# Optimization experiments

Measured on AMD Instinct MI355X. Metric: run time of the kernel, lower is better.

Reference implementation:

```python
import math
import jax, jax.numpy as jnp
import numpy as np

N = 50000      # nodes
E = 800000     # edges
H = 128        # hidden_dim
NR = 16        # num_radial
CUTOFF = 5.0
LN_EPS = 1e-5


def _ln(h, g, b):
    m = jnp.mean(h, axis=-1, keepdims=True)
    v = jnp.mean((h - m) ** 2, axis=-1, keepdims=True)
    return (h - m) * jax.lax.rsqrt(v + LN_EPS) * g + b


def _legendre(angle):
    # degree=4 -> 4 polynomial features
    c = jnp.cos(angle)
    p0 = jnp.ones_like(c)
    p1 = c
    p2 = (3.0 * c * p1 - 1.0 * p0) / 2.0
    p3 = (5.0 * c * p2 - 2.0 * p1) / 3.0
    return jnp.concatenate([p0, p1, p2, p3], axis=-1)


def setup_inputs() -> dict:
    key = jax.random.key(0)
    ks = jax.random.split(key, 16)
    ED = 2 * H + NR + 3  # edge feature dim = 275

    def w(k, shape, fan_in):
        return jax.random.normal(k, shape, jnp.float32) / np.sqrt(fan_in).astype(np.float32)

    return {
        "x": jax.random.normal(ks[0], (N, H), jnp.float32),
        "pos": jax.random.normal(ks[1], (N, 3), jnp.float32),
        "charge": jax.random.normal(ks[2], (N, 1), jnp.float32),
        "edge_attr": jax.random.uniform(ks[3], (E, 4), jnp.float32),
        "edge_index": jax.random.randint(ks[4], (2, E), 0, N),
        "We1": w(ks[5], (ED, H), ED), "be1": jnp.zeros((H,), jnp.float32),
        "g1": jnp.ones((H,), jnp.float32), "bt1": jnp.zeros((H,), jnp.float32),
        "We2": w(ks[6], (H, H), H), "be2": jnp.zeros((H,), jnp.float32),
        "Wn": w(ks[7], (2 * H, H), 2 * H), "bn": jnp.zeros((H,), jnp.float32),
        "gn": jnp.ones((H,), jnp.float32), "btn": jnp.zeros((H,), jnp.float32),
        "Wc1": w(ks[8], (H, H // 2), H), "bc1": jnp.zeros((H // 2,), jnp.float32),
        "Wc2": w(ks[9], (H // 2, 1), H // 2), "bc2": jnp.zeros((1,), jnp.float32),
    }


def reference(x, pos, charge, edge_attr, edge_index,
              We1, be1, g1, bt1, We2, be2, Wn, bn, gn, btn,
              Wc1, bc1, Wc2, bc2):
    src, dst = edge_index[0], edge_index[1]

    rel = pos[dst] - pos[src]                                   # [E,3]
    dist = jnp.sqrt(jnp.sum(rel ** 2, axis=-1, keepdims=True) + 1e-8)
    unit = rel / jnp.clip(dist, 1e-6)

    # edge-attribute gate via Legendre basis of angle/dihedral
    af = _legendre(edge_attr[:, 0:1])
    df = _legendre(edge_attr[:, 1:2])
    a_score = jnp.mean(jnp.abs(af), axis=-1, keepdims=True) * edge_attr[:, 2:3]
    d_score = jnp.mean(jnp.abs(df), axis=-1, keepdims=True) * edge_attr[:, 3:4]
    gate = jnp.clip(1.0 + 0.6 * (a_score + d_score), 0.35, 2.5)  # [E,1]

    # spherical Bessel radial basis
    freq = jnp.arange(1, NR + 1, dtype=jnp.float32) * (math.pi / CUTOFF)
    clipped = jnp.clip(dist, 1e-6)
    rad = jnp.sin(freq * clipped) / clipped                      # [E,NR]

    qs, qd = charge[src], charge[dst]
    ef = jnp.concatenate([
        x[src], x[dst], rad * gate, dist / CUTOFF * gate,
        qs * qd * gate, jnp.abs(qs - qd) * gate], axis=-1)       # [E,275]

    h = jax.nn.silu(ef @ We1 + be1)
    h = _ln(h, g1, bt1)
    eh = jax.nn.silu(h @ We2 + be2)                              # [E,H]

    ones = jnp.ones((eh.shape[0], 1), eh.dtype)
    cnt = jnp.clip(jax.ops.segment_sum(ones, src, num_segments=N), 1.0)
    agg = jax.ops.segment_sum(eh, src, num_segments=N) / cnt     # scatter-mean

    coord = jax.nn.silu(eh @ Wc1 + bc1) @ Wc2 + bc2              # [E,1]
    delta = jax.ops.segment_sum(unit * coord * gate, src, num_segments=N) / cnt

    x_new = x + _ln(jax.nn.silu(jnp.concatenate([x, agg], axis=-1) @ Wn + bn), gn, btn)
    pos_new = pos + 0.1 * delta
    return (x_new, pos_new)
```

## Files before the change

kernel.cpp:

```cpp
#include <hip/hip_runtime.h>
#include <hip/hip_bf16.h>
#include <math.h>


#define HDIM 128
#define GN   16
#define TILE 64
#define HS   136
#define AUXS 32
#define NS   264

#define B_BE1 0
#define B_G1  128
#define B_BT1 256
#define B_BE2 384
#define B_BC1 512
#define B_WC2 576
#define B_BC2 640
#define B_BN  704
#define B_GN  832
#define B_BTN 960
#define BIAS_N 1088

typedef unsigned int uint32;
typedef float f32x4 __attribute__((ext_vector_type(4)));
typedef float f32x2 __attribute__((ext_vector_type(2)));
typedef short short8 __attribute__((ext_vector_type(8)));
typedef unsigned short u16x4 __attribute__((ext_vector_type(4)));

__device__ __forceinline__ float bf2f(__hip_bfloat16 h) { return __bfloat162float(h); }

template<bool BF> __device__ __forceinline__ f32x2 ld2(const void* p, size_t i) {
  if constexpr (BF) {
    uint32 u; __builtin_memcpy(&u, (const char*)p + i * 2, 4);
    f32x2 r; r.x = __uint_as_float(u << 16); r.y = __uint_as_float(u & 0xffff0000u);
    return r;
  } else {
    f32x2 r; __builtin_memcpy(&r, (const char*)p + i * 4, 8);
    return r;
  }
}
template<bool BF> __device__ __forceinline__ float ld1(const void* p, size_t i) {
  if constexpr (BF) {
    __hip_bfloat16 h; __builtin_memcpy(&h, (const char*)p + i * 2, 2);
    return bf2f(h);
  } else {
    float v; __builtin_memcpy(&v, (const char*)p + i * 4, 4);
    return v;
  }
}
template<bool BF> __device__ __forceinline__ void st1(void* p, size_t i, float v) {
  if constexpr (BF) {
    __hip_bfloat16 h = __float2bfloat16(v);
    __builtin_memcpy((char*)p + i * 2, &h, 2);
  } else {
    __builtin_memcpy((char*)p + i * 4, &v, 4);
  }
}

__device__ __forceinline__ unsigned short f2bf(float v) {
  __hip_bfloat16 h = __float2bfloat16(v);
  unsigned short u; __builtin_memcpy(&u, &h, 2);
  return u;
}

template<bool BF> __device__ __forceinline__ f32x4 ld4(const void* p, size_t i) {
  if constexpr (BF) {
    u16x4 u; __builtin_memcpy(&u, (const char*)p + i * 2, 8);
    f32x4 r;
    r.x = __uint_as_float((uint32)u[0] << 16);
    r.y = __uint_as_float((uint32)u[1] << 16);
    r.z = __uint_as_float((uint32)u[2] << 16);
    r.w = __uint_as_float((uint32)u[3] << 16);
    return r;
  } else {
    f32x4 r; __builtin_memcpy(&r, (const char*)p + i * 4, 16);
    return r;
  }
}

template<bool BF> __device__ __forceinline__ short8 ldxrow(const void* x, int row, int col) {
  if constexpr (BF) {
    return *reinterpret_cast<const short8*>((const char*)x + ((size_t)row * HDIM + col) * 2);
  } else {
    const float* p = (const float*)x + (size_t)row * HDIM + col;
    f32x4 v0 = *reinterpret_cast<const f32x4*>(p);
    f32x4 v1 = *reinterpret_cast<const f32x4*>(p + 4);
    short8 a;
    a[0] = (short)f2bf(v0.x); a[1] = (short)f2bf(v0.y);
    a[2] = (short)f2bf(v0.z); a[3] = (short)f2bf(v0.w);
    a[4] = (short)f2bf(v1.x); a[5] = (short)f2bf(v1.y);
    a[6] = (short)f2bf(v1.z); a[7] = (short)f2bf(v1.w);
    return a;
  }
}

__device__ __forceinline__ float silu(float v) { return v / (1.0f + __expf(-v)); }

__device__ __forceinline__ f32x4 splat4(float v) {
  f32x4 r; r.x = v; r.y = v; r.z = v; r.w = v; return r;
}

__device__ __forceinline__ void wave_sync() {
  asm volatile("s_waitcnt lgkmcnt(0)" ::: "memory");
}

__global__ void probe_kernel(const uint32* g1, int* flag) {
  if (threadIdx.x == 0 && blockIdx.x == 0) *flag = (g1[0] == 0x3F800000u) ? 0 : 1;
}

__global__ void hist_kernel(const int* __restrict__ ei, int* __restrict__ cnt, int E) {
  int e = blockIdx.x * 256 + threadIdx.x;
  if (e < E) atomicAdd(&cnt[ei[e]], 1);
}

__global__ void __launch_bounds__(1024) scan_kernel(const int* __restrict__ cnt,
                                                    int* __restrict__ off, int N) {
  __shared__ int part[16];
  __shared__ int carry_s;
  const int t = threadIdx.x;
  const int wid = t >> 6, ln = t & 63;
  if (t == 0) carry_s = 0;
  __syncthreads();
  for (int base = 0; base < N; base += 1024) {
    const int v = (base + t < N) ? cnt[base + t] : 0;
    int inc = v;
#pragma unroll
    for (int s = 1; s < 64; s <<= 1) {
      int u = __shfl_up(inc, s);
      if (ln >= s) inc += u;
    }
    if (ln == 63) part[wid] = inc;
    __syncthreads();
    if (wid == 0) {
      int p = (ln < 16) ? part[ln] : 0;
#pragma unroll
      for (int s = 1; s < 16; s <<= 1) {
        int u = __shfl_up(p, s);
        if (ln >= s) p += u;
      }
      if (ln < 16) part[ln] = p;
    }
    __syncthreads();
    const int woff = (wid > 0) ? part[wid - 1] : 0;
    const int carry = carry_s;
    if (base + t < N) off[base + t] = carry + inc + woff - v;
    __syncthreads();
    if (t == 1023) carry_s = carry + part[15];
    __syncthreads();
  }
  if (t == 0) off[N] = carry_s;
}

__global__ void fill_kernel(const int* __restrict__ ei, const int* __restrict__ off,
                            int* __restrict__ cursor, int* __restrict__ eidx, int E) {
  int e = blockIdx.x * 256 + threadIdx.x;
  if (e < E) {
    int s = ei[e];
    int p = atomicAdd(&cursor[s], 1);
    eidx[off[s] + p] = e;
  }
}

template<bool BF>
__global__ void __launch_bounds__(256) prep_kernel(
    const void* __restrict__ x,
    const void* __restrict__ pos, const void* __restrict__ charge,
    const void* __restrict__ We1, const void* __restrict__ We2,
    const void* __restrict__ Wc1, const void* __restrict__ Wn,
    const void* __restrict__ be1, const void* __restrict__ g1,
    const void* __restrict__ bt1, const void* __restrict__ be2,
    const void* __restrict__ bc1, const void* __restrict__ wc2,
    const void* __restrict__ bc2, const void* __restrict__ bn,
    const void* __restrict__ gn, const void* __restrict__ btn,
    const int* __restrict__ flag,
    float* __restrict__ posf, float* __restrict__ chgf, float* __restrict__ biasf,
    __hip_bfloat16* __restrict__ WT1, __hip_bfloat16* __restrict__ WT2,
    __hip_bfloat16* __restrict__ WTc1, __hip_bfloat16* __restrict__ WTn,
    __hip_bfloat16* __restrict__ xbf,
    int N) {
  if (*flag != (BF ? 1 : 0)) return;
  const int gt = blockIdx.x * 256 + threadIdx.x;
  const int gs = gridDim.x * 256;
  for (int i = gt; i < N * 3; i += gs) posf[i] = ld1<BF>(pos, i);
  for (int i = gt; i < N; i += gs) chgf[i] = ld1<BF>(charge, i);
  if (xbf) {
    for (int i = gt; i < N * HDIM; i += gs) xbf[i] = __float2bfloat16(ld1<BF>(x, i));
  }
  for (int i = gt; i < 128; i += gs) {
    biasf[B_BE1 + i] = ld1<BF>(be1, i);
    biasf[B_G1  + i] = ld1<BF>(g1, i);
    biasf[B_BT1 + i] = ld1<BF>(bt1, i);
    biasf[B_BE2 + i] = ld1<BF>(be2, i);
    biasf[B_BN  + i] = ld1<BF>(bn, i);
    biasf[B_GN  + i] = ld1<BF>(gn, i);
    biasf[B_BTN + i] = ld1<BF>(btn, i);
  }
  for (int i = gt; i < 64; i += gs) {
    biasf[B_BC1 + i] = ld1<BF>(bc1, i);
    biasf[B_WC2 + i] = ld1<BF>(wc2, i);
  }
  if (gt == 0) biasf[B_BC2] = ld1<BF>(bc2, 0);
  for (int i = gt; i < 128 * 288; i += gs) {
    int n = i / 288, k = i % 288;
    float v = (k < 275) ? ld1<BF>(We1, (size_t)k * 128 + n) : 0.f;
    WT1[i] = __float2bfloat16(v);
  }
  for (int i = gt; i < 128 * 128; i += gs) {
    int n = i / 128, k = i % 128;
    WT2[i] = __float2bfloat16(ld1<BF>(We2, (size_t)k * 128 + n));
  }
  for (int i = gt; i < 64 * 128; i += gs) {
    int n = i / 128, k = i % 128;
    WTc1[i] = __float2bfloat16(ld1<BF>(Wc1, (size_t)k * 64 + n));
  }
  for (int i = gt; i < 128 * 256; i += gs) {
    int n = i / 256, k = i % 256;
    WTn[i] = __float2bfloat16(ld1<BF>(Wn, (size_t)k * 128 + n));
  }
}

template<bool BF, bool XB>
__global__ void __launch_bounds__(256, 2) edge_mfma_kernel(
    const void* __restrict__ x, const void* __restrict__ eattr,
    const int* __restrict__ ei,
    const int* __restrict__ off, const int* __restrict__ eidx,
    const int* __restrict__ flag,
    const float* __restrict__ posf, const float* __restrict__ chgf,
    const float* __restrict__ biasf,
    const __hip_bfloat16* __restrict__ WT1, const __hip_bfloat16* __restrict__ WT2,
    const __hip_bfloat16* __restrict__ WTc1, const __hip_bfloat16* __restrict__ WTn,
    const __hip_bfloat16* __restrict__ xbf,
    void* __restrict__ out, int N, int E) {
  if (*flag != (BF ? 1 : 0)) return;

  __shared__ __align__(16) __hip_bfloat16 hbuf[4 * 16 * HS];
  __shared__ __align__(16) __hip_bfloat16 aux_s[TILE * AUXS];
  __shared__ float base_s[GN * 132];
  __shared__ float agg_s[(GN + 1) * 132];
  __shared__ float dsum_s[(GN + 1) * 4];
  __shared__ float sgate[TILE];
  __shared__ float sunit[TILE * 3];
  __shared__ int sdst_s[TILE];
  __shared__ int offs[GN + 1];
  __shared__ short ssrc16[TILE];

  const int tid = threadIdx.x;
  const int w = tid >> 6;
  const int lane = tid & 63;
  const int g0 = blockIdx.x * GN;
  const int c16 = lane & 15;
  const int g4 = lane >> 4;

  for (int i = tid; i < (GN + 1) * 132; i += 256) agg_s[i] = 0.f;
  for (int i = tid; i < (GN + 1) * 4; i += 256) dsum_s[i] = 0.f;
  if (tid <= GN) {
    int node = g0 + tid;
    offs[tid] = off[node < N ? node : N];
  }
  __syncthreads();

  const int eStart = offs[0];
  const int eEnd = offs[GN];
  const int ntiles = (eEnd - eStart + TILE - 1) / TILE;

  __hip_bfloat16* hw = hbuf + (size_t)w * 16 * HS;

  const short* WT1s = reinterpret_cast<const short*>(WT1);
  const short* WT2s = reinterpret_cast<const short*>(WT2);
  const short* WTc1s = reinterpret_cast<const short*>(WTc1);
  const short* xbs = reinterpret_cast<const short*>(xbf);

  {
    for (int i = tid; i < GN * 32; i += 256) {
      const int row = i >> 5, c4 = (i & 31) * 4;
      int node = g0 + row; node = (node < N) ? node : (N - 1);
      if constexpr (XB) {
        *reinterpret_cast<u16x4*>(&hbuf[row * HS + c4]) =
            *reinterpret_cast<const u16x4*>(&xbs[(size_t)node * HDIM + c4]);
      } else {
        const size_t xb = (size_t)node * HDIM + c4;
        f32x2 v0 = ld2<BF>(x, xb);
        f32x2 v1 = ld2<BF>(x, xb + 2);
        u16x4 pk;
        pk[0] = f2bf(v0.x); pk[1] = f2bf(v0.y); pk[2] = f2bf(v1.x); pk[3] = f2bf(v1.y);
        *reinterpret_cast<u16x4*>(&hbuf[row * HS + c4]) = pk;
      }
    }
    __syncthreads();
    f32x4 acc2[2];
#pragma unroll
    for (int j = 0; j < 2; j++)
      acc2[j] = splat4(biasf[B_BE1 + (2 * w + j) * 16 + c16]);
#pragma unroll
    for (int ks = 0; ks < 4; ks++) {
      short8 a = *reinterpret_cast<const short8*>(&hbuf[c16 * HS + ks * 32 + g4 * 8]);
#pragma unroll
      for (int j = 0; j < 2; j++) {
        const int nt = 2 * w + j;
        short8 b = *reinterpret_cast<const short8*>(
            &WT1s[(size_t)(nt * 16 + c16) * 288 + ks * 32 + g4 * 8]);
        acc2[j] = __builtin_amdgcn_mfma_f32_16x16x32_bf16(a, b, acc2[j], 0, 0, 0);
      }
    }
#pragma unroll
    for (int j = 0; j < 2; j++) {
      const int nt = 2 * w + j;
#pragma unroll
      for (int r = 0; r < 4; r++)
        base_s[(g4 * 4 + r) * 132 + nt * 16 + c16] = acc2[j][r];
    }
    __syncthreads();
  }

  const float FSC = 3.14159265358979323846f / 5.0f;

  const int es_pl = lane >> 2;
  int pos_cur = eStart + w * 16 + es_pl;
  bool v_cur = (ntiles > 0) && (pos_cur < eEnd);
  int eg_cur = v_cur ? eidx[pos_cur] : 0;
  int dst_cur = v_cur ? ei[(size_t)E + eg_cur] : g0;

  for (int t = 0; t < ntiles; t++) {
    const int pos_nx = pos_cur + TILE;
    const bool v_nx = pos_nx < eEnd;
    const int eg_nx = v_nx ? eidx[pos_nx] : 0;

    {
      const int es = es_pl, sub = lane & 3, slot = w * 16 + es;
      const bool valid = v_cur;
      int loc = GN;
      if (valid) {
        loc = 0;
#pragma unroll
        for (int st = 8; st > 0; st >>= 1)
          if (loc + st <= GN - 1 && offs[loc + st] <= pos_cur) loc += st;
      }
      const int dstn = dst_cur;
      float gate = 0.f, dcl = 1.f, ux = 0.f, uy = 0.f, uz = 0.f;
      float f0 = 0.f, f1 = 0.f, f2 = 0.f;
      if (valid && sub == 0) {
        const int srcg = g0 + loc;
        const float px = posf[3 * srcg + 0], py = posf[3 * srcg + 1], pz = posf[3 * srcg + 2];
        const float qn = chgf[srcg];
        const float dx = posf[3 * dstn + 0] - px;
        const float dy = posf[3 * dstn + 1] - py;
        const float dz = posf[3 * dstn + 2] - pz;
        const float dist = sqrtf(dx * dx + dy * dy + dz * dz + 1e-8f);
        dcl = fmaxf(dist, 1e-6f);
        ux = dx / dcl; uy = dy / dcl; uz = dz / dcl;
        f32x4 ea = ld4<BF>(eattr, (size_t)eg_cur * 4);
        const float ca = __cosf(ea.x);
        const float p2a = 0.5f * (3.f * ca * ca - 1.f);
        const float p3a = (5.f * ca * p2a - 2.f * ca) * (1.f / 3.f);
        const float ma = 0.25f * (1.f + fabsf(ca) + fabsf(p2a) + fabsf(p3a));
        const float cd = __cosf(ea.y);
        const float p2d = 0.5f * (3.f * cd * cd - 1.f);
        const float p3d = (5.f * cd * p2d - 2.f * cd) * (1.f / 3.f);
        const float md = 0.25f * (1.f + fabsf(cd) + fabsf(p2d) + fabsf(p3d));
        gate = fminf(fmaxf(1.f + 0.6f * (ma * ea.z + md * ea.w), 0.35f), 2.5f);
        const float qd = chgf[dstn];
        f0 = dist * 0.2f * gate;
        f1 = qn * qd * gate;
        f2 = fabsf(qn - qd) * gate;
      }
      const int bl = lane & ~3;
      dcl = __shfl(dcl, bl);
      gate = __shfl(gate, bl);
      u16x4 rv;
#pragma unroll
      for (int i = 0; i < 4; i++) {
        const float k1 = (float)(sub * 4 + i + 1);
        rv[i] = f2bf(__sinf(FSC * k1 * dcl) / dcl * gate);
      }
      *reinterpret_cast<u16x4*>(&aux_s[slot * AUXS + sub * 4]) = rv;
      if (sub == 0) {
        sgate[slot] = gate;
        ssrc16[slot] = (short)(valid ? loc : GN);
        sdst_s[slot] = dstn;
        sunit[slot * 3 + 0] = ux; sunit[slot * 3 + 1] = uy;
        sunit[slot * 3 + 2] = uz;
        u16x4 ev;
        ev[0] = f2bf(f0); ev[1] = f2bf(f1); ev[2] = f2bf(f2); ev[3] = 0;
        *reinterpret_cast<u16x4*>(&aux_s[slot * AUXS + 16]) = ev;
      } else {
        u16x4 z; z[0] = 0; z[1] = 0; z[2] = 0; z[3] = 0;
        *reinterpret_cast<u16x4*>(&aux_s[slot * AUXS + 16 + sub * 4]) = z;
      }
    }
    wave_sync();

    int ssr[4];
#pragma unroll
    for (int r = 0; r < 4; r++) ssr[r] = (int)ssrc16[w * 16 + g4 * 4 + r];
    const int dstc = sdst_s[w * 16 + c16];

    f32x4 acc[8];
#pragma unroll
    for (int nt = 0; nt < 8; nt++) {
      f32x4 c;
#pragma unroll
      for (int r = 0; r < 4; r++) {
        const int sb = (ssr[r] < GN) ? ssr[r] : (GN - 1);
        c[r] = base_s[sb * 132 + nt * 16 + c16];
      }
      acc[nt] = c;
    }
#pragma unroll
    for (int ks = 0; ks < 4; ks++) {
      short8 a;
      if constexpr (XB) {
        a = *reinterpret_cast<const short8*>(
            &xbs[(size_t)dstc * HDIM + ks * 32 + g4 * 8]);
      } else {
        a = ldxrow<BF>(x, dstc, ks * 32 + g4 * 8);
      }
#pragma unroll
      for (int nt = 0; nt < 8; nt++) {
        short8 b = *reinterpret_cast<const short8*>(
            &WT1s[(size_t)(nt * 16 + c16) * 288 + 128 + ks * 32 + g4 * 8]);
        acc[nt] = __builtin_amdgcn_mfma_f32_16x16x32_bf16(a, b, acc[nt], 0, 0, 0);
      }
    }
    {
      short8 a = *reinterpret_cast<const short8*>(&aux_s[(w * 16 + c16) * AUXS + g4 * 8]);
#pragma unroll
      for (int nt = 0; nt < 8; nt++) {
        short8 b = *reinterpret_cast<const short8*>(
            &WT1s[(size_t)(nt * 16 + c16) * 288 + 256 + g4 * 8]);
        acc[nt] = __builtin_amdgcn_mfma_f32_16x16x32_bf16(a, b, acc[nt], 0, 0, 0);
      }
    }

    {
      float sm[4] = {0.f, 0.f, 0.f, 0.f}, sq[4] = {0.f, 0.f, 0.f, 0.f};
#pragma unroll
      for (int nt = 0; nt < 8; nt++)
#pragma unroll
        for (int r = 0; r < 4; r++) {
          const float v = silu(acc[nt][r]);
          acc[nt][r] = v;
          sm[r] += v;
          sq[r] += v * v;
        }
#pragma unroll
      for (int r = 0; r < 4; r++) {
#pragma unroll
        for (int mk = 1; mk <= 8; mk <<= 1) {
          sm[r] += __shfl_xor(sm[r], mk);
          sq[r] += __shfl_xor(sq[r], mk);
        }
      }
      float mu[4], rsd[4];
#pragma unroll
      for (int r = 0; r < 4; r++) {
        mu[r] = sm[r] * (1.f / HDIM);
        const float var = sq[r] * (1.f / HDIM) - mu[r] * mu[r];
        rsd[r] = rsqrtf(var + 1e-5f);
      }
#pragma unroll
      for (int nt = 0; nt < 8; nt++) {
        const float gg = biasf[B_G1 + nt * 16 + c16];
        const float bb = biasf[B_BT1 + nt * 16 + c16];
#pragma unroll
        for (int r = 0; r < 4; r++) {
          const int m = g4 * 4 + r;
          hw[m * HS + nt * 16 + c16] =
              __float2bfloat16((acc[nt][r] - mu[r]) * rsd[r] * gg + bb);
        }
      }
    }
    wave_sync();

#pragma unroll
    for (int nt = 0; nt < 8; nt++) acc[nt] = splat4(biasf[B_BE2 + nt * 16 + c16]);
#pragma unroll
    for (int ks = 0; ks < 4; ks++) {
      short8 a = *reinterpret_cast<const short8*>(&hw[c16 * HS + ks * 32 + g4 * 8]);
#pragma unroll
      for (int nt = 0; nt < 8; nt++) {
        short8 b = *reinterpret_cast<const short8*>(
            &WT2s[(size_t)(nt * 16 + c16) * 128 + ks * 32 + g4 * 8]);
        acc[nt] = __builtin_amdgcn_mfma_f32_16x16x32_bf16(a, b, acc[nt], 0, 0, 0);
      }
    }
#pragma unroll
    for (int nt = 0; nt < 8; nt++)
#pragma unroll
      for (int r = 0; r < 4; r++) {
        const float v = silu(acc[nt][r]);
        const int m = g4 * 4 + r;
        hw[m * HS + nt * 16 + c16] = __float2bfloat16(v);
        atomicAdd(&agg_s[ssr[r] * 132 + nt * 16 + c16], v);
      }
    wave_sync();

    {
      f32x4 a3[4];
#pragma unroll
      for (int q = 0; q < 4; q++) a3[q] = splat4(biasf[B_BC1 + q * 16 + c16]);
#pragma unroll
      for (int ks = 0; ks < 4; ks++) {
        short8 a = *reinterpret_cast<const short8*>(&hw[c16 * HS + ks * 32 + g4 * 8]);
#pragma unroll
        for (int q = 0; q < 4; q++) {
          short8 b = *reinterpret_cast<const short8*>(
              &WTc1s[(size_t)(q * 16 + c16) * 128 + ks * 32 + g4 * 8]);
          a3[q] = __builtin_amdgcn_mfma_f32_16x16x32_bf16(a, b, a3[q], 0, 0, 0);
        }
      }
      float cp[4] = {0.f, 0.f, 0.f, 0.f};
#pragma unroll
      for (int q = 0; q < 4; q++) {
        const float wv = biasf[B_WC2 + q * 16 + c16];
#pragma unroll
        for (int r = 0; r < 4; r++) cp[r] += silu(a3[q][r]) * wv;
      }
#pragma unroll
      for (int r = 0; r < 4; r++) {
#pragma unroll
        for (int mk = 1; mk <= 8; mk <<= 1) cp[r] += __shfl_xor(cp[r], mk);
      }
      const float bc2v = biasf[B_BC2];
      if (c16 < 4) {
        const int r = c16;
        const int slot = w * 16 + g4 * 4 + r;
        const float cr = (r == 0) ? cp[0] : (r == 1) ? cp[1] : (r == 2) ? cp[2] : cp[3];
        const float scale = (cr + bc2v) * sgate[slot];
        const int sl = (int)ssrc16[slot];
        atomicAdd(&dsum_s[sl * 4 + 0], sunit[slot * 3 + 0] * scale);
        atomicAdd(&dsum_s[sl * 4 + 1], sunit[slot * 3 + 1] * scale);
        atomicAdd(&dsum_s[sl * 4 + 2], sunit[slot * 3 + 2] * scale);
      }
    }
    wave_sync();

    const int dst_nx = v_nx ? ei[(size_t)E + eg_nx] : g0;
    pos_cur = pos_nx;
    v_cur = v_nx;
    eg_cur = eg_nx;
    dst_cur = dst_nx;
  }
  __syncthreads();

  for (int m = w; m < GN; m += 4) {
    const int node = g0 + m;
    const bool nv = node < N;
    const int dg = nv ? (offs[m + 1] - offs[m]) : 0;
    const float inv = 1.f / fmaxf((float)dg, 1.f);
    const int cb = lane * 4;
    u16x4 pk;
    if (nv && cb < 128) {
      if constexpr (XB) {
        pk = *reinterpret_cast<const u16x4*>(&xbs[(size_t)node * HDIM + cb]);
      } else {
#pragma unroll
        for (int j = 0; j < 4; j++) pk[j] = f2bf(ld1<BF>(x, (size_t)node * HDIM + cb + j));
      }
    } else {
#pragma unroll
      for (int j = 0; j < 4; j++) {
        const int col = cb + j;
        float v = 0.f;
        if (nv && col >= 128) v = agg_s[m * 132 + (col - 128)] * inv;
        pk[j] = f2bf(v);
      }
    }
    *reinterpret_cast<u16x4*>(&hbuf[m * NS + cb]) = pk;
  }
  __syncthreads();

  if (w == 0) {
    const short* WTns = reinterpret_cast<const short*>(WTn);
    f32x4 an[8];
#pragma unroll
    for (int nt = 0; nt < 8; nt++) an[nt] = splat4(biasf[B_BN + nt * 16 + c16]);
#pragma unroll
    for (int ks = 0; ks < 8; ks++) {
      short8 a = *reinterpret_cast<const short8*>(&hbuf[c16 * NS + ks * 32 + g4 * 8]);
#pragma unroll
      for (int nt = 0; nt < 8; nt++) {
        short8 b = *reinterpret_cast<const short8*>(
            &WTns[(size_t)(nt * 16 + c16) * 256 + ks * 32 + g4 * 8]);
        an[nt] = __builtin_amdgcn_mfma_f32_16x16x32_bf16(a, b, an[nt], 0, 0, 0);
      }
    }
    float sm[4] = {0.f, 0.f, 0.f, 0.f}, sq[4] = {0.f, 0.f, 0.f, 0.f};
#pragma unroll
    for (int nt = 0; nt < 8; nt++)
#pragma unroll
      for (int r = 0; r < 4; r++) {
        const float v = silu(an[nt][r]);
        an[nt][r] = v;
        sm[r] += v;
        sq[r] += v * v;
      }
#pragma unroll
    for (int r = 0; r < 4; r++) {
#pragma unroll
      for (int mk = 1; mk <= 8; mk <<= 1) {
        sm[r] += __shfl_xor(sm[r], mk);
        sq[r] += __shfl_xor(sq[r], mk);
      }
    }
    float mu[4], rsd[4];
#pragma unroll
    for (int r = 0; r < 4; r++) {
      mu[r] = sm[r] * (1.f / HDIM);
      const float var = sq[r] * (1.f / HDIM) - mu[r] * mu[r];
      rsd[r] = rsqrtf(var + 1e-5f);
    }
#pragma unroll
    for (int nt = 0; nt < 8; nt++) {
      const float gg = biasf[B_GN + nt * 16 + c16];
      const float bb = biasf[B_BTN + nt * 16 + c16];
#pragma unroll
      for (int r = 0; r < 4; r++) {
        const int m = g4 * 4 + r;
        const int node = g0 + m;
        if (node < N) {
          const int col = nt * 16 + c16;
          const float xo = ld1<BF>(x, (size_t)node * HDIM + col);
          st1<BF>(out, (size_t)node * HDIM + col,
                  xo + (an[nt][r] - mu[r]) * rsd[r] * gg + bb);
        }
      }
    }
    if (lane < GN) {
      const int node = g0 + lane;
      if (node < N) {
        const int dg = offs[lane + 1] - offs[lane];
        const float inv = 1.f / fmaxf((float)dg, 1.f);
#pragma unroll
        for (int d = 0; d < 3; d++) {
          const float pv = posf[(size_t)node * 3 + d] + 0.1f * dsum_s[lane * 4 + d] * inv;
          st1<BF>(out, (size_t)N * HDIM + (size_t)node * 3 + d, pv);
        }
      }
    }
  }
}

extern "C" void kernel_launch(void* const* d_in, const int* in_sizes, int n_in,
                              void* d_out, int out_size, void* d_ws, size_t ws_size,
                              hipStream_t stream) {
  const void* x      = d_in[0];
  const void* pos    = d_in[1];
  const void* charge = d_in[2];
  const void* eattr  = d_in[3];
  const int*  ei     = (const int*)d_in[4];
  const void* We1 = d_in[5];  const void* be1 = d_in[6];
  const void* g1  = d_in[7];  const void* bt1 = d_in[8];
  const void* We2 = d_in[9];  const void* be2 = d_in[10];
  const void* Wn  = d_in[11]; const void* bn  = d_in[12];
  const void* gn  = d_in[13]; const void* btn = d_in[14];
  const void* Wc1 = d_in[15]; const void* bc1 = d_in[16];
  const void* Wc2 = d_in[17]; const void* bc2 = d_in[18];

  const int N = in_sizes[0] / HDIM;
  const int E = in_sizes[3] / 4;

  int* wsI    = (int*)d_ws;
  int* flag   = wsI;
  int* cnt    = wsI + 1;
  int* cursor = cnt + N;
  int* off    = cursor + N;
  int* eidx   = off + (N + 1);

  char* base = (char*)d_ws;
  size_t o = ((size_t)(3 * N + 2 + E) * 4 + 511) & ~(size_t)511;
  float* posf = (float*)(base + o);
  o = (o + (size_t)N * 3 * 4 + 511) & ~(size_t)511;
  float* chgf = (float*)(base + o);
  o = (o + (size_t)N * 4 + 511) & ~(size_t)511;
  float* biasf = (float*)(base + o);
  o = (o + (size_t)BIAS_N * 4 + 511) & ~(size_t)511;
  __hip_bfloat16* WT1 = (__hip_bfloat16*)(base + o);
  o = (o + (size_t)128 * 288 * 2 + 511) & ~(size_t)511;
  __hip_bfloat16* WT2 = (__hip_bfloat16*)(base + o);
  o = (o + (size_t)128 * 128 * 2 + 511) & ~(size_t)511;
  __hip_bfloat16* WTc1 = (__hip_bfloat16*)(base + o);
  o = (o + (size_t)64 * 128 * 2 + 511) & ~(size_t)511;
  __hip_bfloat16* WTn = (__hip_bfloat16*)(base + o);
  o = (o + (size_t)128 * 256 * 2 + 511) & ~(size_t)511;
  __hip_bfloat16* xbf_ws = (__hip_bfloat16*)(base + o);
  const bool xb_fits = (o + (size_t)N * HDIM * 2) <= ws_size;

  hipMemsetAsync(d_ws, 0, (size_t)(1 + 2 * N) * sizeof(int), stream);

  probe_kernel<<<1, 64, 0, stream>>>((const uint32*)g1, flag);

  const int eb = (E + 255) / 256;
  hist_kernel<<<eb, 256, 0, stream>>>(ei, cnt, E);
  scan_kernel<<<1, 1024, 0, stream>>>(cnt, off, N);
  fill_kernel<<<eb, 256, 0, stream>>>(ei, off, cursor, eidx, E);

  prep_kernel<true><<<512, 256, 0, stream>>>(
      x, pos, charge, We1, We2, Wc1, Wn, be1, g1, bt1, be2, bc1, Wc2, bc2, bn, gn, btn,
      flag, posf, chgf, biasf, WT1, WT2, WTc1, WTn, nullptr, N);
  prep_kernel<false><<<512, 256, 0, stream>>>(
      x, pos, charge, We1, We2, Wc1, Wn, be1, g1, bt1, be2, bc1, Wc2, bc2, bn, gn, btn,
      flag, posf, chgf, biasf, WT1, WT2, WTc1, WTn, xb_fits ? xbf_ws : nullptr, N);

  const int nb = (N + GN - 1) / GN;
  edge_mfma_kernel<true, true><<<nb, 256, 0, stream>>>(
      x, eattr, ei, off, eidx, flag, posf, chgf, biasf, WT1, WT2, WTc1, WTn,
      (const __hip_bfloat16*)x, d_out, N, E);
  if (xb_fits) {
    edge_mfma_kernel<false, true><<<nb, 256, 0, stream>>>(
        x, eattr, ei, off, eidx, flag, posf, chgf, biasf, WT1, WT2, WTc1, WTn,
        xbf_ws, d_out, N, E);
  } else {
    edge_mfma_kernel<false, false><<<nb, 256, 0, stream>>>(
        x, eattr, ei, off, eidx, flag, posf, chgf, biasf, WT1, WT2, WTc1, WTn,
        nullptr, d_out, N, E);
  }
}
```

Measured before the change: 1.365 ms.

## Parallelize CSR offset scan and pass edge metadata via shuffles instead of LDS

The single-block sequential prefix scan over node counts is replaced by a three-kernel multi-block scan: per-block scans, a scan of the block sums, then adding the block offsets back. In the edge kernel, each edge's source node is read directly from the edge index instead of being found by binary search over the offsets. Destination and local-source indices are broadcast with wave shuffles instead of going through shared memory. Edge attributes are prefetched one tile ahead, and the explicit waitcnt barriers are removed. This trades two extra kernel launches and a few extra global loads for less serial scan time and fewer LDS round-trips, and relies on the removed waitcnts not being needed for correctness of LDS reuse within a wave.

```diff
diff --git a/kernel.cpp b/kernel.cpp
--- a/kernel.cpp
+++ b/kernel.cpp
@@ -101,10 +101,6 @@
   f32x4 r; r.x = v; r.y = v; r.z = v; r.w = v; return r;
 }
 
-__device__ __forceinline__ void wave_sync() {
-  asm volatile("s_waitcnt lgkmcnt(0)" ::: "memory");
-}
-
 __global__ void probe_kernel(const uint32* g1, int* flag) {
   if (threadIdx.x == 0 && blockIdx.x == 0) *flag = (g1[0] == 0x3F800000u) ? 0 : 1;
 }
@@ -114,42 +110,69 @@
   if (e < E) atomicAdd(&cnt[ei[e]], 1);
 }
 
-__global__ void __launch_bounds__(1024) scan_kernel(const int* __restrict__ cnt,
-                                                    int* __restrict__ off, int N) {
+__global__ void __launch_bounds__(1024) scan1_kernel(const int* __restrict__ cnt,
+                                                     int* __restrict__ off,
+                                                     int* __restrict__ bsum, int N) {
   __shared__ int part[16];
-  __shared__ int carry_s;
-  const int t = threadIdx.x;
-  const int wid = t >> 6, ln = t & 63;
-  if (t == 0) carry_s = 0;
+  const int t = threadIdx.x, wid = t >> 6, ln = t & 63;
+  const int i = blockIdx.x * 1024 + t;
+  const int v = (i < N) ? cnt[i] : 0;
+  int inc = v;
+#pragma unroll
+  for (int s = 1; s < 64; s <<= 1) {
+    int u = __shfl_up(inc, s);
+    if (ln >= s) inc += u;
+  }
+  if (ln == 63) part[wid] = inc;
   __syncthreads();
-  for (int base = 0; base < N; base += 1024) {
-    const int v = (base + t < N) ? cnt[base + t] : 0;
-    int inc = v;
-#pragma unroll
-    for (int s = 1; s < 64; s <<= 1) {
-      int u = __shfl_up(inc, s);
-      if (ln >= s) inc += u;
-    }
-    if (ln == 63) part[wid] = inc;
-    __syncthreads();
-    if (wid == 0) {
-      int p = (ln < 16) ? part[ln] : 0;
-#pragma unroll
-      for (int s = 1; s < 16; s <<= 1) {
-        int u = __shfl_up(p, s);
-        if (ln >= s) p += u;
-      }
-      if (ln < 16) part[ln] = p;
-    }
-    __syncthreads();
-    const int woff = (wid > 0) ? part[wid - 1] : 0;
-    const int carry = carry_s;
-    if (base + t < N) off[base + t] = carry + inc + woff - v;
-    __syncthreads();
-    if (t == 1023) carry_s = carry + part[15];
-    __syncthreads();
-  }
-  if (t == 0) off[N] = carry_s;
+  if (wid == 0 && ln < 16) {
+    int p = part[ln];
+#pragma unroll
+    for (int s = 1; s < 16; s <<= 1) {
+      int u = __shfl_up(p, s);
+      if (ln >= s) p += u;
+    }
+    part[ln] = p;
+  }
+  __syncthreads();
+  const int woff = (wid > 0) ? part[wid - 1] : 0;
+  if (i < N) off[i] = woff + inc - v;
+  if (t == 0) bsum[blockIdx.x] = part[15];
+}
+
+__global__ void __launch_bounds__(1024) scan2_kernel(int* __restrict__ bsum,
+                                                     int* __restrict__ off,
+                                                     int NB, int N) {
+  __shared__ int part[16];
+  const int t = threadIdx.x, wid = t >> 6, ln = t & 63;
+  const int v = (t < NB) ? bsum[t] : 0;
+  int inc = v;
+#pragma unroll
+  for (int s = 1; s < 64; s <<= 1) {
+    int u = __shfl_up(inc, s);
+    if (ln >= s) inc += u;
+  }
+  if (ln == 63) part[wid] = inc;
+  __syncthreads();
+  if (wid == 0 && ln < 16) {
+    int p = part[ln];
+#pragma unroll
+    for (int s = 1; s < 16; s <<= 1) {
+      int u = __shfl_up(p, s);
+      if (ln >= s) p += u;
+    }
+    part[ln] = p;
+  }
+  __syncthreads();
+  const int woff = (wid > 0) ? part[wid - 1] : 0;
+  if (t < NB) bsum[t] = woff + inc - v;
+  if (t == 0) off[N] = part[15];
+}
+
+__global__ void __launch_bounds__(1024) scan3_kernel(int* __restrict__ off,
+                                                     const int* __restrict__ bsum, int N) {
+  const int i = blockIdx.x * 1024 + threadIdx.x;
+  if (i < N) off[i] += bsum[blockIdx.x];
 }
 
 __global__ void fill_kernel(const int* __restrict__ ei, const int* __restrict__ off,
@@ -241,7 +264,6 @@
   __shared__ float dsum_s[(GN + 1) * 4];
   __shared__ float sgate[TILE];
   __shared__ float sunit[TILE * 3];
-  __shared__ int sdst_s[TILE];
   __shared__ int offs[GN + 1];
   __shared__ short ssrc16[TILE];
 
@@ -316,31 +338,32 @@
   const float FSC = 3.14159265358979323846f / 5.0f;
 
   const int es_pl = lane >> 2;
+  const int sub = lane & 3;
   int pos_cur = eStart + w * 16 + es_pl;
   bool v_cur = (ntiles > 0) && (pos_cur < eEnd);
-  int eg_cur = v_cur ? eidx[pos_cur] : 0;
-  int dst_cur = v_cur ? ei[(size_t)E + eg_cur] : g0;
+  int eg0 = v_cur ? eidx[pos_cur] : 0;
+  int src_cur = v_cur ? ei[eg0] : g0;
+  int dst_cur = v_cur ? ei[(size_t)E + eg0] : g0;
+  f32x4 ea_cur = ld4<BF>(eattr, (size_t)eg0 * 4);
 
   for (int t = 0; t < ntiles; t++) {
     const int pos_nx = pos_cur + TILE;
     const bool v_nx = pos_nx < eEnd;
     const int eg_nx = v_nx ? eidx[pos_nx] : 0;
 
+    const int dstc = __shfl(dst_cur, c16 << 2);
+    const int loc_own = v_cur ? (src_cur - g0) : GN;
+    int ssr[4];
+#pragma unroll
+    for (int r = 0; r < 4; r++) ssr[r] = __shfl(loc_own, ((g4 << 2) + r) << 2);
+
     {
-      const int es = es_pl, sub = lane & 3, slot = w * 16 + es;
-      const bool valid = v_cur;
-      int loc = GN;
-      if (valid) {
-        loc = 0;
-#pragma unroll
-        for (int st = 8; st > 0; st >>= 1)
-          if (loc + st <= GN - 1 && offs[loc + st] <= pos_cur) loc += st;
-      }
-      const int dstn = dst_cur;
+      const int slot = w * 16 + es_pl;
       float gate = 0.f, dcl = 1.f, ux = 0.f, uy = 0.f, uz = 0.f;
       float f0 = 0.f, f1 = 0.f, f2 = 0.f;
-      if (valid && sub == 0) {
-        const int srcg = g0 + loc;
+      if (v_cur && sub == 0) {
+        const int srcg = src_cur;
+        const int dstn = dst_cur;
         const float px = posf[3 * srcg + 0], py = posf[3 * srcg + 1], pz = posf[3 * srcg + 2];
         const float qn = chgf[srcg];
         const float dx = posf[3 * dstn + 0] - px;
@@ -349,16 +372,15 @@
         const float dist = sqrtf(dx * dx + dy * dy + dz * dz + 1e-8f);
         dcl = fmaxf(dist, 1e-6f);
         ux = dx / dcl; uy = dy / dcl; uz = dz / dcl;
-        f32x4 ea = ld4<BF>(eattr, (size_t)eg_cur * 4);
-        const float ca = __cosf(ea.x);
+        const float ca = __cosf(ea_cur.x);
         const float p2a = 0.5f * (3.f * ca * ca - 1.f);
         const float p3a = (5.f * ca * p2a - 2.f * ca) * (1.f / 3.f);
         const float ma = 0.25f * (1.f + fabsf(ca) + fabsf(p2a) + fabsf(p3a));
-        const float cd = __cosf(ea.y);
+        const float cd = __cosf(ea_cur.y);
         const float p2d = 0.5f * (3.f * cd * cd - 1.f);
         const float p3d = (5.f * cd * p2d - 2.f * cd) * (1.f / 3.f);
         const float md = 0.25f * (1.f + fabsf(cd) + fabsf(p2d) + fabsf(p3d));
-        gate = fminf(fmaxf(1.f + 0.6f * (ma * ea.z + md * ea.w), 0.35f), 2.5f);
+        gate = fminf(fmaxf(1.f + 0.6f * (ma * ea_cur.z + md * ea_cur.w), 0.35f), 2.5f);
         const float qd = chgf[dstn];
         f0 = dist * 0.2f * gate;
         f1 = qn * qd * gate;
@@ -376,8 +398,7 @@
       *reinterpret_cast<u16x4*>(&aux_s[slot * AUXS + sub * 4]) = rv;
       if (sub == 0) {
         sgate[slot] = gate;
-        ssrc16[slot] = (short)(valid ? loc : GN);
-        sdst_s[slot] = dstn;
+        ssrc16[slot] = (short)loc_own;
         sunit[slot * 3 + 0] = ux; sunit[slot * 3 + 1] = uy;
         sunit[slot * 3 + 2] = uz;
         u16x4 ev;
@@ -388,12 +409,6 @@
         *reinterpret_cast<u16x4*>(&aux_s[slot * AUXS + 16 + sub * 4]) = z;
       }
     }
-    wave_sync();
-
-    int ssr[4];
-#pragma unroll
-    for (int r = 0; r < 4; r++) ssr[r] = (int)ssrc16[w * 16 + g4 * 4 + r];
-    const int dstc = sdst_s[w * 16 + c16];
 
     f32x4 acc[8];
 #pragma unroll
@@ -470,7 +485,6 @@
         }
       }
     }
-    wave_sync();
 
 #pragma unroll
     for (int nt = 0; nt < 8; nt++) acc[nt] = splat4(biasf[B_BE2 + nt * 16 + c16]);
@@ -493,7 +507,6 @@
         hw[m * HS + nt * 16 + c16] = __float2bfloat16(v);
         atomicAdd(&agg_s[ssr[r] * 132 + nt * 16 + c16], v);
       }
-    wave_sync();
 
     {
       f32x4 a3[4];
@@ -533,13 +546,15 @@
         atomicAdd(&dsum_s[sl * 4 + 2], sunit[slot * 3 + 2] * scale);
       }
     }
-    wave_sync();
-
+
+    const int src_nx = v_nx ? ei[eg_nx] : g0;
     const int dst_nx = v_nx ? ei[(size_t)E + eg_nx] : g0;
+    const f32x4 ea_nx = ld4<BF>(eattr, (size_t)eg_nx * 4);
     pos_cur = pos_nx;
     v_cur = v_nx;
-    eg_cur = eg_nx;
+    src_cur = src_nx;
     dst_cur = dst_nx;
+    ea_cur = ea_nx;
   }
   __syncthreads();
 
@@ -659,6 +674,7 @@
 
   const int N = in_sizes[0] / HDIM;
   const int E = in_sizes[3] / 4;
+  const int NB = (N + 1023) / 1024;
 
   int* wsI    = (int*)d_ws;
   int* flag   = wsI;
@@ -666,9 +682,10 @@
   int* cursor = cnt + N;
   int* off    = cursor + N;
   int* eidx   = off + (N + 1);
+  int* bsum   = eidx + E;
 
   char* base = (char*)d_ws;
-  size_t o = ((size_t)(3 * N + 2 + E) * 4 + 511) & ~(size_t)511;
+  size_t o = ((size_t)(3 * N + 2 + E + 1024) * 4 + 511) & ~(size_t)511;
   float* posf = (float*)(base + o);
   o = (o + (size_t)N * 3 * 4 + 511) & ~(size_t)511;
   float* chgf = (float*)(base + o);
@@ -692,7 +709,9 @@
 
   const int eb = (E + 255) / 256;
   hist_kernel<<<eb, 256, 0, stream>>>(ei, cnt, E);
-  scan_kernel<<<1, 1024, 0, stream>>>(cnt, off, N);
+  scan1_kernel<<<NB, 1024, 0, stream>>>(cnt, off, bsum, N);
+  scan2_kernel<<<1, 1024, 0, stream>>>(bsum, off, NB, N);
+  scan3_kernel<<<NB, 1024, 0, stream>>>(off, bsum, N);
   fill_kernel<<<eb, 256, 0, stream>>>(ei, off, cursor, eidx, E);
 
   prep_kernel<true><<<512, 256, 0, stream>>>(
```

After: 1.868 ms. 36.8% more time.
